# Optimization experiments

Measured on AMD Instinct MI355X. Metric: run time of the kernel, lower is better.

The kernel has to match this reference:

```python
import jax, jax.numpy as jnp
import numpy as np
from functools import partial

D_MODEL = 1024
D_HIDDEN = 4096
N_BLOCKS = 4
D_VOCAB = 32000
BATCH = 2
SEQ = 2048
LN_EPS = 1e-5
LRELU_SLOPE = 0.01  # torch nn.LeakyReLU default


def setup_inputs() -> dict:
    key = jax.random.key(0)
    ks = jax.random.split(key, 16)
    d, h, L, v = D_MODEL, D_HIDDEN, N_BLOCKS, D_VOCAB
    scale = d ** 0.5
    inp = {
        "tokens": jax.random.randint(ks[0], (BATCH, SEQ), 0, v, dtype=jnp.int64)
                  if jax.config.jax_enable_x64 else
                  jax.random.randint(ks[0], (BATCH, SEQ), 0, v, dtype=jnp.int32),
        "emb": jax.random.normal(ks[1], (v, d), jnp.float32) * 0.02,
        # per-block stacked params (leading axis = layer) for lax.scan
        "qk": jax.random.normal(ks[2], (L, d, d), jnp.float32) / scale,
        "ov": jax.random.normal(ks[3], (L, d, d), jnp.float32) / scale,
        "w_up": jax.random.normal(ks[4], (L, d, h), jnp.float32) / scale,
        "b_up": jnp.zeros((L, h), jnp.float32),
        "w_hid": jax.random.normal(ks[5], (L, h, h), jnp.float32) / (h ** 0.5),
        "b_hid": jnp.zeros((L, h), jnp.float32),
        "w_down": jax.random.normal(ks[6], (L, h, d), jnp.float32) / (h ** 0.5),
        "b_down": jnp.zeros((L, d), jnp.float32),
        "ln1_g": jnp.ones((L, d), jnp.float32),
        "ln1_b": jnp.zeros((L, d), jnp.float32),
        "ln2_g": jnp.ones((L, d), jnp.float32),
        "ln2_b": jnp.zeros((L, d), jnp.float32),
    }
    return inp


def _layer_norm(x, g, b):
    mu = jnp.mean(x, axis=-1, keepdims=True)
    var = jnp.mean(jnp.square(x - mu), axis=-1, keepdims=True)
    return (x - mu) * jax.lax.rsqrt(var + LN_EPS) * g + b


def _forward(tokens, emb, qk, ov, w_up, b_up, w_hid, b_hid, w_down, b_down,
             ln1_g, ln1_b, ln2_g, ln2_b):
    x = emb[tokens]                                   # [B, S, D]
    seq = tokens.shape[1]
    scale = jnp.asarray(D_MODEL ** 0.5, x.dtype)
    causal = jnp.tril(jnp.ones((seq, seq), bool))     # True = keep

    def block(x, p):
        (qk, ov, w_up, b_up, w_hid, b_hid, w_down, b_down,
         g1, b1, g2, b2) = p
        h = _layer_norm(x, g1, b1)
        # attention: (h @ qk @ h^T) / sqrt(d), causal mask, softmax, @ h @ ov
        scores = jnp.einsum('bsd,de,bte->bst', h, qk, h) / scale
        scores = jnp.where(causal, scores, -jnp.inf)
        attn = jax.nn.softmax(scores, axis=-1)
        x = x + jnp.einsum('bst,btd,de->bse', attn, h, ov)
        # MLP with LeakyReLU after every layer (incl. output)
        m = _layer_norm(x, g2, b2)
        m = jax.nn.leaky_relu(m @ w_up + b_up, LRELU_SLOPE)
        m = jax.nn.leaky_relu(m @ w_hid + b_hid, LRELU_SLOPE)
        m = jax.nn.leaky_relu(m @ w_down + b_down, LRELU_SLOPE)
        return x + m, None

    params = (qk, ov, w_up, b_up, w_hid, b_hid, w_down, b_down,
              ln1_g, ln1_b, ln2_g, ln2_b)
    x, _ = jax.lax.scan(block, x, params)
    return x @ emb.T                                  # [B, S, V] logits


@jax.jit
def reference(tokens, emb, qk, ov, w_up, b_up, w_hid, b_hid, w_down, b_down,
              ln1_g, ln1_b, ln2_g, ln2_b):
    return _forward(tokens, emb, qk, ov, w_up, b_up, w_hid, b_hid,
                    w_down, b_down, ln1_g, ln1_b, ln2_g, ln2_b)
```

## Files before the change

kernel.cpp:

```cpp
#include <hip/hip_runtime.h>

#define BS   4096
#define SEQL 2048
#define DM   1024
#define DH   4096
#define NV   32000

using u16 = unsigned short;

typedef __attribute__((ext_vector_type(8))) short bf16x8;
typedef __attribute__((ext_vector_type(4))) float f32x4;

__device__ __forceinline__ u16 f2b(float f) {
  union { float f; unsigned u; } c; c.f = f;
  unsigned u = c.u;
  u = (u + 0x7FFFu + ((u >> 16) & 1u)) >> 16;
  return (u16)u;
}

__device__ __forceinline__ void gld16(const u16* g, u16* l) {
  __builtin_amdgcn_global_load_lds(
      (__attribute__((address_space(1))) void*)(void*)const_cast<u16*>(g),
      (__attribute__((address_space(3))) void*)l, 16, 0, 0);
}

__global__ __launch_bounds__(256) void k_embed(const int* __restrict__ tok,
                                               const float* __restrict__ emb,
                                               float* __restrict__ x) {
  const long row = blockIdx.x;
  const long e = tok[row];
  ((float4*)(x + row * DM))[threadIdx.x] = ((const float4*)(emb + e * DM))[threadIdx.x];
}

__global__ __launch_bounds__(256) void k_cvt(const float* __restrict__ in,
                                             u16* __restrict__ out, int n4) {
  int i = blockIdx.x * 256 + threadIdx.x;
  if (i < n4) {
    float4 v = ((const float4*)in)[i];
    ushort4 o;
    o.x = f2b(v.x); o.y = f2b(v.y); o.z = f2b(v.z); o.w = f2b(v.w);
    ((ushort4*)out)[i] = o;
  }
}

__global__ __launch_bounds__(256) void k_ln(const float* __restrict__ x,
                                            const float* __restrict__ g,
                                            const float* __restrict__ b,
                                            u16* __restrict__ out) {
  const long row = blockIdx.x;
  const int t = threadIdx.x;
  float4 v = ((const float4*)(x + row * DM))[t];
  float s  = v.x + v.y + v.z + v.w;
  float q2 = v.x*v.x + v.y*v.y + v.z*v.z + v.w*v.w;
#pragma unroll
  for (int o = 1; o < 64; o <<= 1) { s += __shfl_xor(s, o); q2 += __shfl_xor(q2, o); }
  __shared__ float rs_[4], rq_[4];
  const int lane = t & 63, wid = t >> 6;
  if (lane == 0) { rs_[wid] = s; rq_[wid] = q2; }
  __syncthreads();
  s  = rs_[0] + rs_[1] + rs_[2] + rs_[3];
  q2 = rq_[0] + rq_[1] + rq_[2] + rq_[3];
  const float mu   = s * (1.f / 1024.f);
  const float var  = q2 * (1.f / 1024.f) - mu * mu;
  const float rstd = rsqrtf(var + 1e-5f);
  float4 gg = ((const float4*)g)[t];
  float4 bb = ((const float4*)b)[t];
  ushort4 o;
  o.x = f2b((v.x - mu) * rstd * gg.x + bb.x);
  o.y = f2b((v.y - mu) * rstd * gg.y + bb.y);
  o.z = f2b((v.z - mu) * rstd * gg.z + bb.z);
  o.w = f2b((v.w - mu) * rstd * gg.w + bb.w);
  ((ushort4*)(out + row * DM))[t] = o;
}

__device__ __forceinline__ u16 to_b16(float v) { return f2b(v); }
__device__ __forceinline__ u16 to_b16(u16 v)   { return v; }

template <typename T>
__global__ __launch_bounds__(256) void k_transpose(const T* __restrict__ in,
                                                   u16* __restrict__ out,
                                                   int R, int C, long inz, long outz) {
  __shared__ u16 tile[32][33];
  const T* ip = in + (long)blockIdx.z * inz;
  u16* op = out + (long)blockIdx.z * outz;
  const int tx = threadIdx.x & 31, ty = threadIdx.x >> 5;
  const long c0 = (long)blockIdx.x * 32, r0 = (long)blockIdx.y * 32;
#pragma unroll
  for (int i = 0; i < 4; ++i)
    tile[ty + i * 8][tx] = to_b16(ip[(r0 + ty + i * 8) * C + c0 + tx]);
  __syncthreads();
#pragma unroll
  for (int i = 0; i < 4; ++i)
    op[(c0 + ty + i * 8) * R + r0 + tx] = tile[tx][ty + i * 8];
}

__global__ __launch_bounds__(256) void k_softmax(const float* __restrict__ sc,
                                                 u16* __restrict__ at) {
  const int r = blockIdx.x;
  const long z = blockIdx.y;
  const int t = threadIdx.x;
  const float* row = sc + (z * SEQL + r) * SEQL;
  u16* orow = at + (z * SEQL + r) * SEQL;
  float vals[8];
  float mx = -3.4e38f;
#pragma unroll
  for (int i = 0; i < 8; ++i) {
    int c = i * 256 + t;
    float v = (c <= r) ? row[c] : -3.4e38f;
    vals[i] = v;
    mx = fmaxf(mx, v);
  }
#pragma unroll
  for (int o = 1; o < 64; o <<= 1) mx = fmaxf(mx, __shfl_xor(mx, o));
  __shared__ float rm[4], rsum[4];
  const int lane = t & 63, wid = t >> 6;
  if (lane == 0) rm[wid] = mx;
  __syncthreads();
  mx = fmaxf(fmaxf(rm[0], rm[1]), fmaxf(rm[2], rm[3]));
  float sum = 0.f;
#pragma unroll
  for (int i = 0; i < 8; ++i) {
    int c = i * 256 + t;
    float e = (c <= r) ? __expf(vals[i] - mx) : 0.f;
    vals[i] = e;
    sum += e;
  }
#pragma unroll
  for (int o = 1; o < 64; o <<= 1) sum += __shfl_xor(sum, o);
  if (lane == 0) rsum[wid] = sum;
  __syncthreads();
  sum = rsum[0] + rsum[1] + rsum[2] + rsum[3];
  const float inv = 1.f / sum;
#pragma unroll
  for (int i = 0; i < 8; ++i) orow[i * 256 + t] = f2b(vals[i] * inv);
}

template <int EPI, bool BIAS, bool LRELU>
__global__ __launch_bounds__(256, 2) void k_gemm_bt(
    const u16* __restrict__ A, const u16* __restrict__ B, void* __restrict__ C,
    const float* __restrict__ bias, int K, int N,
    long sAz, long sBz, long sCz, float scale) {
  __shared__ u16 lA[128 * 32];
  __shared__ u16 lB[128 * 32];
  const int t = threadIdx.x;
  const long z = blockIdx.z;
  const long row0 = (long)blockIdx.x * 128;
  const long col0 = (long)blockIdx.y * 128;
  const u16* Ab = A + z * sAz;
  const u16* Bb = B + z * sBz;

  const int rr = t >> 2;
  const int c8 = (t & 3) * 8;
  const u16* gA0 = Ab + (row0 + rr) * K + c8;
  const u16* gA1 = Ab + (row0 + 64 + rr) * K + c8;
  const u16* gB0 = Bb + (col0 + rr) * K + c8;
  const u16* gB1 = Bb + (col0 + 64 + rr) * K + c8;
  u16* sA0 = &lA[rr * 32 + c8];
  u16* sA1 = &lA[(64 + rr) * 32 + c8];
  u16* sB0 = &lB[rr * 32 + c8];
  u16* sB1 = &lB[(64 + rr) * 32 + c8];

  const int lane = t & 63;
  const int w = t >> 6;
  const int wr = (w >> 1) * 64, wc = (w & 1) * 64;
  const int fr = lane & 15;
  const int fk = (lane >> 4) * 8;

  f32x4 acc[4][4] = {};

  for (int k0 = 0; k0 < K; k0 += 32) {
    gld16(gA0 + k0, sA0);
    gld16(gA1 + k0, sA1);
    gld16(gB0 + k0, sB0);
    gld16(gB1 + k0, sB1);
    __syncthreads();
    bf16x8 av[4], bv[4];
#pragma unroll
    for (int m = 0; m < 4; ++m) av[m] = *(const bf16x8*)&lA[(wr + m * 16 + fr) * 32 + fk];
#pragma unroll
    for (int n = 0; n < 4; ++n) bv[n] = *(const bf16x8*)&lB[(wc + n * 16 + fr) * 32 + fk];
#pragma unroll
    for (int m = 0; m < 4; ++m)
#pragma unroll
      for (int n = 0; n < 4; ++n)
        acc[m][n] = __builtin_amdgcn_mfma_f32_16x16x32_bf16(av[m], bv[n], acc[m][n], 0, 0, 0);
    __syncthreads();
  }

  const int er = (lane >> 4) * 4;
  const int ec = lane & 15;
#pragma unroll
  for (int m = 0; m < 4; ++m) {
#pragma unroll
    for (int n = 0; n < 4; ++n) {
#pragma unroll
      for (int j = 0; j < 4; ++j) {
        long r = row0 + wr + m * 16 + er + j;
        long c = col0 + wc + n * 16 + ec;
        float v = acc[m][n][j] * scale;
        if (BIAS)  v += bias[c];
        if (LRELU) v = v > 0.f ? v : 0.01f * v;
        if (EPI == 0)      ((float*)C)[z * sCz + r * (long)N + c] = v;
        else if (EPI == 1) ((u16*)C)[z * sCz + r * (long)N + c] = f2b(v);
        else               ((float*)C)[z * sCz + r * (long)N + c] += v;
      }
    }
  }
}

extern "C" void kernel_launch(void* const* d_in, const int* in_sizes, int n_in,
                              void* d_out, int out_size, void* d_ws, size_t ws_size,
                              hipStream_t stream) {
  const int*   tokens = (const int*)d_in[0];
  const float* emb    = (const float*)d_in[1];
  const float* qk     = (const float*)d_in[2];
  const float* ov     = (const float*)d_in[3];
  const float* wup    = (const float*)d_in[4];
  const float* bup    = (const float*)d_in[5];
  const float* whid   = (const float*)d_in[6];
  const float* bhid   = (const float*)d_in[7];
  const float* wdown  = (const float*)d_in[8];
  const float* bdown  = (const float*)d_in[9];
  const float* g1     = (const float*)d_in[10];
  const float* b1     = (const float*)d_in[11];
  const float* g2     = (const float*)d_in[12];
  const float* b2     = (const float*)d_in[13];

  char* Ob = (char*)d_out;
  float* scores = (float*)(Ob + 0);
  u16*   attn   = (u16*)(Ob + 33554432);
  u16*   m1     = (u16*)(Ob + 50331648);
  u16*   m2     = (u16*)(Ob + 83886080);
  u16*   qkT    = (u16*)(Ob + 117440512);
  u16*   ovT    = qkT + 1048576;
  u16*   upT    = ovT + 1048576;
  u16*   hidT   = upT + 4194304;
  u16*   downT  = hidT + 16777216;
  float* xres   = (float*)(Ob + 171966464);
  u16*   h      = (u16*)(Ob + 188743680);
  u16*   hT     = (u16*)(Ob + 197132288);
  u16*   q      = (u16*)(Ob + 205520896);
  u16*   attnV  = (u16*)(Ob + 213909504);

  u16* embB = (u16*)d_ws;
  u16* xB   = (u16*)((char*)d_ws + 65536000);

  k_embed<<<dim3(BS), 256, 0, stream>>>(tokens, emb, xres);
  k_cvt<<<dim3(32000), 256, 0, stream>>>(emb, embB, 8192000);

  for (int l = 0; l < 4; ++l) {
    k_transpose<float><<<dim3(32, 32, 1),  256, 0, stream>>>(qk    + (long)l * 1048576,  qkT,   1024, 1024, 0, 0);
    k_transpose<float><<<dim3(32, 32, 1),  256, 0, stream>>>(ov    + (long)l * 1048576,  ovT,   1024, 1024, 0, 0);
    k_transpose<float><<<dim3(128, 32, 1), 256, 0, stream>>>(wup   + (long)l * 4194304,  upT,   1024, 4096, 0, 0);
    k_transpose<float><<<dim3(128, 128, 1),256, 0, stream>>>(whid  + (long)l * 16777216, hidT,  4096, 4096, 0, 0);
    k_transpose<float><<<dim3(32, 128, 1), 256, 0, stream>>>(wdown + (long)l * 4194304,  downT, 4096, 1024, 0, 0);

    k_ln<<<dim3(BS), 256, 0, stream>>>(xres, g1 + l * 1024, b1 + l * 1024, h);
    k_transpose<u16><<<dim3(32, 64, 2), 256, 0, stream>>>(h, hT, 2048, 1024, 2048L * 1024, 1024L * 2048);
    k_gemm_bt<1, false, false><<<dim3(32, 8, 1), 256, 0, stream>>>(
        h, qkT, q, nullptr, 1024, 1024, 0, 0, 0, 0.03125f);
    k_gemm_bt<0, false, false><<<dim3(16, 16, 2), 256, 0, stream>>>(
        q, h, scores, nullptr, 1024, 2048, 2048L * 1024, 2048L * 1024, 2048L * 2048, 1.f);
    k_softmax<<<dim3(2048, 2), 256, 0, stream>>>(scores, attn);
    k_gemm_bt<1, false, false><<<dim3(16, 8, 2), 256, 0, stream>>>(
        attn, hT, attnV, nullptr, 2048, 1024, 2048L * 2048, 1024L * 2048, 2048L * 1024, 1.f);
    k_gemm_bt<2, false, false><<<dim3(32, 8, 1), 256, 0, stream>>>(
        attnV, ovT, xres, nullptr, 1024, 1024, 0, 0, 0, 1.f);

    k_ln<<<dim3(BS), 256, 0, stream>>>(xres, g2 + l * 1024, b2 + l * 1024, h);
    k_gemm_bt<1, true, true><<<dim3(32, 32, 1), 256, 0, stream>>>(
        h, upT, m1, bup + l * 4096, 1024, 4096, 0, 0, 0, 1.f);
    k_gemm_bt<1, true, true><<<dim3(32, 32, 1), 256, 0, stream>>>(
        m1, hidT, m2, bhid + l * 4096, 4096, 4096, 0, 0, 0, 1.f);
    k_gemm_bt<2, true, true><<<dim3(32, 8, 1), 256, 0, stream>>>(
        m2, downT, xres, bdown + l * 1024, 4096, 1024, 0, 0, 0, 1.f);
  }

  k_cvt<<<dim3(4096), 256, 0, stream>>>(xres, xB, 1048576);
  k_gemm_bt<0, false, false><<<dim3(32, 250, 1), 256, 0, stream>>>(
      xB, embB, (float*)d_out, nullptr, 1024, 32000, 0, 0, 0, 1.f);
}
```

Baseline: 2.270 ms.

## Skip masked causal tiles, batch weight transposes, swizzle vocab GEMM blocks

The scores GEMM now returns early for tiles entirely above the causal diagonal. The attn·h GEMM limits its K loop to the nonzero causal prefix of each row tile. All layers' weight transposes run once before the loop as batched launches into enlarged scratch regions, replacing per-layer launches. The large vocab projection also remaps block indices so neighbouring blocks share data in L2. This relies on softmax writing exact zeros in masked positions and on the larger scratch layout fitting in the output buffer.

Result: slower. 2.379 ms (+4.8%).

```diff
diff --git a/kernel.cpp b/kernel.cpp
--- a/kernel.cpp
+++ b/kernel.cpp
@@ -135,7 +135,7 @@
   for (int i = 0; i < 8; ++i) orow[i * 256 + t] = f2b(vals[i] * inv);
 }
 
-template <int EPI, bool BIAS, bool LRELU>
+template <int EPI, bool BIAS, bool LRELU, int CAUSAL, bool SWZ>
 __global__ __launch_bounds__(256, 2) void k_gemm_bt(
     const u16* __restrict__ A, const u16* __restrict__ B, void* __restrict__ C,
     const float* __restrict__ bias, int K, int N,
@@ -144,8 +144,18 @@
   __shared__ u16 lB[128 * 32];
   const int t = threadIdx.x;
   const long z = blockIdx.z;
-  const long row0 = (long)blockIdx.x * 128;
-  const long col0 = (long)blockIdx.y * 128;
+  int bx = blockIdx.x, by = blockIdx.y;
+  if (SWZ) {
+    int id = bx + gridDim.x * by;
+    int cpx = (gridDim.x * gridDim.y) >> 3;
+    int s = (id & 7) * cpx + (id >> 3);
+    bx = s % gridDim.x;
+    by = s / gridDim.x;
+  }
+  const long row0 = (long)bx * 128;
+  const long col0 = (long)by * 128;
+  if (CAUSAL == 1 && col0 > row0 + 127) return;
+  const int Klim = (CAUSAL == 2) ? min(K, (int)row0 + 128) : K;
   const u16* Ab = A + z * sAz;
   const u16* Bb = B + z * sBz;
 
@@ -168,7 +178,7 @@
 
   f32x4 acc[4][4] = {};
 
-  for (int k0 = 0; k0 < K; k0 += 32) {
+  for (int k0 = 0; k0 < Klim; k0 += 32) {
     gld16(gA0 + k0, sA0);
     gld16(gA1 + k0, sA1);
     gld16(gB0 + k0, sB0);
@@ -232,15 +242,15 @@
   u16*   m1     = (u16*)(Ob + 50331648);
   u16*   m2     = (u16*)(Ob + 83886080);
   u16*   qkT    = (u16*)(Ob + 117440512);
-  u16*   ovT    = qkT + 1048576;
-  u16*   upT    = ovT + 1048576;
-  u16*   hidT   = upT + 4194304;
-  u16*   downT  = hidT + 16777216;
-  float* xres   = (float*)(Ob + 171966464);
-  u16*   h      = (u16*)(Ob + 188743680);
-  u16*   hT     = (u16*)(Ob + 197132288);
-  u16*   q      = (u16*)(Ob + 205520896);
-  u16*   attnV  = (u16*)(Ob + 213909504);
+  u16*   ovT    = (u16*)(Ob + 125829120);
+  u16*   upT    = (u16*)(Ob + 134217728);
+  u16*   hidT   = (u16*)(Ob + 167772160);
+  u16*   downT  = (u16*)(Ob + 301989888);
+  float* xres   = (float*)(Ob + 335544320);
+  u16*   h      = (u16*)(Ob + 352321536);
+  u16*   hT     = (u16*)(Ob + 360710144);
+  u16*   q      = (u16*)(Ob + 369098752);
+  u16*   attnV  = (u16*)(Ob + 377487360);
 
   u16* embB = (u16*)d_ws;
   u16* xB   = (u16*)((char*)d_ws + 65536000);
@@ -248,35 +258,35 @@
   k_embed<<<dim3(BS), 256, 0, stream>>>(tokens, emb, xres);
   k_cvt<<<dim3(32000), 256, 0, stream>>>(emb, embB, 8192000);
 
+  k_transpose<float><<<dim3(32, 32, 4),   256, 0, stream>>>(qk,    qkT,   1024, 1024, 1048576,  1048576);
+  k_transpose<float><<<dim3(32, 32, 4),   256, 0, stream>>>(ov,    ovT,   1024, 1024, 1048576,  1048576);
+  k_transpose<float><<<dim3(128, 32, 4),  256, 0, stream>>>(wup,   upT,   1024, 4096, 4194304,  4194304);
+  k_transpose<float><<<dim3(128, 128, 4), 256, 0, stream>>>(whid,  hidT,  4096, 4096, 16777216, 16777216);
+  k_transpose<float><<<dim3(32, 128, 4),  256, 0, stream>>>(wdown, downT, 4096, 1024, 4194304,  4194304);
+
   for (int l = 0; l < 4; ++l) {
-    k_transpose<float><<<dim3(32, 32, 1),  256, 0, stream>>>(qk    + (long)l * 1048576,  qkT,   1024, 1024, 0, 0);
-    k_transpose<float><<<dim3(32, 32, 1),  256, 0, stream>>>(ov    + (long)l * 1048576,  ovT,   1024, 1024, 0, 0);
-    k_transpose<float><<<dim3(128, 32, 1), 256, 0, stream>>>(wup   + (long)l * 4194304,  upT,   1024, 4096, 0, 0);
-    k_transpose<float><<<dim3(128, 128, 1),256, 0, stream>>>(whid  + (long)l * 16777216, hidT,  4096, 4096, 0, 0);
-    k_transpose<float><<<dim3(32, 128, 1), 256, 0, stream>>>(wdown + (long)l * 4194304,  downT, 4096, 1024, 0, 0);
-
     k_ln<<<dim3(BS), 256, 0, stream>>>(xres, g1 + l * 1024, b1 + l * 1024, h);
     k_transpose<u16><<<dim3(32, 64, 2), 256, 0, stream>>>(h, hT, 2048, 1024, 2048L * 1024, 1024L * 2048);
-    k_gemm_bt<1, false, false><<<dim3(32, 8, 1), 256, 0, stream>>>(
-        h, qkT, q, nullptr, 1024, 1024, 0, 0, 0, 0.03125f);
-    k_gemm_bt<0, false, false><<<dim3(16, 16, 2), 256, 0, stream>>>(
+    k_gemm_bt<1, false, false, 0, false><<<dim3(32, 8, 1), 256, 0, stream>>>(
+        h, qkT + (long)l * 1048576, q, nullptr, 1024, 1024, 0, 0, 0, 0.03125f);
+    k_gemm_bt<0, false, false, 1, false><<<dim3(16, 16, 2), 256, 0, stream>>>(
         q, h, scores, nullptr, 1024, 2048, 2048L * 1024, 2048L * 1024, 2048L * 2048, 1.f);
     k_softmax<<<dim3(2048, 2), 256, 0, stream>>>(scores, attn);
-    k_gemm_bt<1, false, false><<<dim3(16, 8, 2), 256, 0, stream>>>(
+    k_gemm_bt<1, false, false, 2, false><<<dim3(16, 8, 2), 256, 0, stream>>>(
         attn, hT, attnV, nullptr, 2048, 1024, 2048L * 2048, 1024L * 2048, 2048L * 1024, 1.f);
-    k_gemm_bt<2, false, false><<<dim3(32, 8, 1), 256, 0, stream>>>(
-        attnV, ovT, xres, nullptr, 1024, 1024, 0, 0, 0, 1.f);
+    k_gemm_bt<2, false, false, 0, false><<<dim3(32, 8, 1), 256, 0, stream>>>(
+        attnV, ovT + (long)l * 1048576, xres, nullptr, 1024, 1024, 0, 0, 0, 1.f);
 
     k_ln<<<dim3(BS), 256, 0, stream>>>(xres, g2 + l * 1024, b2 + l * 1024, h);
-    k_gemm_bt<1, true, true><<<dim3(32, 32, 1), 256, 0, stream>>>(
-        h, upT, m1, bup + l * 4096, 1024, 4096, 0, 0, 0, 1.f);
-    k_gemm_bt<1, true, true><<<dim3(32, 32, 1), 256, 0, stream>>>(
-        m1, hidT, m2, bhid + l * 4096, 4096, 4096, 0, 0, 0, 1.f);
-    k_gemm_bt<2, true, true><<<dim3(32, 8, 1), 256, 0, stream>>>(
-        m2, downT, xres, bdown + l * 1024, 4096, 1024, 0, 0, 0, 1.f);
+    k_gemm_bt<1, true, true, 0, false><<<dim3(32, 32, 1), 256, 0, stream>>>(
+        h, upT + (long)l * 4194304, m1, bup + l * 4096, 1024, 4096, 0, 0, 0, 1.f);
+    k_gemm_bt<1, true, true, 0, false><<<dim3(32, 32, 1), 256, 0, stream>>>(
+        m1, hidT + (long)l * 16777216, m2, bhid + l * 4096, 4096, 4096, 0, 0, 0, 1.f);
+    k_gemm_bt<2, true, true, 0, false><<<dim3(32, 8, 1), 256, 0, stream>>>(
+        m2, downT + (long)l * 4194304, xres, bdown + l * 1024, 4096, 1024, 0, 0, 0, 1.f);
   }
 
   k_cvt<<<dim3(4096), 256, 0, stream>>>(xres, xB, 1048576);
-  k_gemm_bt<0, false, false><<<dim3(32, 250, 1), 256, 0, stream>>>(
+  k_gemm_bt<0, false, false, 0, true><<<dim3(32, 250, 1), 256, 0, stream>>>(
       xB, embB, (float*)d_out, nullptr, 1024, 32000, 0, 0, 0, 1.f);
 }
```
